# Optimization experiments

Measured on AMD Instinct MI355X. Metric: run time of the kernel, lower is better.

The kernel has to match this reference:

```python
import jax, jax.numpy as jnp
import numpy as np
from jax import lax

B, NC, NF = 16, 1024, 4096   # clouds, coarse pts/cloud, fine pts/cloud
C_IN, C_SKIP, C_HID, K = 256, 128, 256, 3
BN_EPS = 1e-5


def setup_inputs() -> dict:
    key = jax.random.key(0)
    ks = jax.random.split(key, 12)
    inp = {
        "x": jax.random.normal(ks[0], (B * NC, C_IN), jnp.float32),
        "pos": jax.random.normal(ks[1], (B * NC, 3), jnp.float32),
        "batch": jnp.arange(B * NC, dtype=jnp.int64) // NC,
        "x_skip": jax.random.normal(ks[2], (B * NF, C_SKIP), jnp.float32),
        "pos_skip": jax.random.normal(ks[3], (B * NF, 3), jnp.float32),
        "batch_skip": jnp.arange(B * NF, dtype=jnp.int64) // NF,
    }
    d_in = C_IN + C_SKIP
    inp["W1"] = jax.random.normal(ks[4], (d_in, C_HID), jnp.float32) / np.sqrt(d_in)
    inp["b1"] = jnp.zeros((C_HID,), jnp.float32)
    inp["g1"] = jnp.ones((C_HID,), jnp.float32)
    inp["be1"] = jnp.zeros((C_HID,), jnp.float32)
    inp["W2"] = jax.random.normal(ks[5], (C_HID, C_HID), jnp.float32) / np.sqrt(C_HID)
    inp["b2"] = jnp.zeros((C_HID,), jnp.float32)
    inp["g2"] = jnp.ones((C_HID,), jnp.float32)
    inp["be2"] = jnp.zeros((C_HID,), jnp.float32)
    return inp


def _knn_interpolate(x, pos, pos_skip):
    # batches are contiguous equal-size -> reshape per cloud
    xb = x.reshape(B, NC, C_IN)
    pc = pos.reshape(B, NC, 3)
    pf = pos_skip.reshape(B, NF, 3)
    # squared distances [B, NF, NC]
    d2 = jnp.sum((pf[:, :, None, :] - pc[:, None, :, :]) ** 2, axis=-1)
    neg_d, idx = lax.top_k(-d2, K)                      # [B, NF, K]
    w = 1.0 / jnp.maximum(-neg_d, 1e-16)                # inverse-squared-distance weights
    feats = xb[jnp.arange(B)[:, None, None], idx]       # [B, NF, K, C_IN]
    out = jnp.sum(w[..., None] * feats, axis=2) / jnp.sum(w, axis=2, keepdims=True)
    return out.reshape(B * NF, C_IN)


def _mlp_layer(h, W, b, g, be):
    z = jax.nn.relu(h @ W + b)
    mean = jnp.mean(z, axis=0)
    var = jnp.mean((z - mean) ** 2, axis=0)            # biased var, as torch BN
    return (z - mean) * lax.rsqrt(var + BN_EPS) * g + be


def reference(x, pos, batch, x_skip, pos_skip, batch_skip,
              W1, b1, g1, be1, W2, b2, g2, be2):
    h = _knn_interpolate(x, pos, pos_skip)
    h = jnp.concatenate([h, x_skip], axis=1)            # [B*NF, C_IN+C_SKIP]
    h = _mlp_layer(h, W1, b1, g1, be1)
    h = _mlp_layer(h, W2, b2, g2, be2)
    return h
```

## Files before the change

kernel.cpp:

```cpp
#include <hip/hip_runtime.h>
#include <hip/hip_bf16.h>
#include <hip/hip_cooperative_groups.h>

namespace cg = cooperative_groups;

#define NB    16
#define NC    1024
#define NF    4096
#define MROWS 65536
#define CIN   256
#define CSK   128
#define DIN   384
#define CHID  256
#define BN_EPS 1e-5f

typedef __attribute__((ext_vector_type(8))) short bf16x8;
typedef __attribute__((ext_vector_type(4))) float f32x4;

__device__ __forceinline__ unsigned short f2bfu(float f) {
  __hip_bfloat16 h = __float2bfloat16(f);
  return __builtin_bit_cast(unsigned short, h);
}
__device__ __forceinline__ float bfu2f(unsigned short u) {
  unsigned int w = ((unsigned int)u) << 16;
  return __builtin_bit_cast(float, w);
}

__device__ __forceinline__ void load_lds16(const void* g, void* lds) {
  __builtin_amdgcn_global_load_lds(
      (const __attribute__((address_space(1))) unsigned int*)g,
      (__attribute__((address_space(3))) unsigned int*)lds, 16, 0, 0);
}

__device__ __forceinline__ void ins3(float d2, int j, float& b0, float& b1,
                                     float& b2v, int& i0, int& i1, int& i2) {
  const bool c0 = d2 < b0, c1 = d2 < b1, c2 = d2 < b2v;
  const float nb1 = __builtin_amdgcn_fmed3f(d2, b0, b1);
  const float nb2 = __builtin_amdgcn_fmed3f(d2, b1, b2v);
  i2  = c1 ? i1 : (c2 ? j : i2);
  i1  = c0 ? i0 : (c1 ? j : i1);
  i0  = c0 ? j : i0;
  b2v = nb2;
  b1  = nb1;
  b0  = fminf(d2, b0);
}

__device__ __forceinline__ void ins3tb(float d, int j, float& b0, float& b1,
                                       float& b2v, int& i0, int& i1, int& i2) {
  const bool c0 = (d < b0) || (d == b0 && j < i0);
  const bool c1 = (d < b1) || (d == b1 && j < i1);
  const bool c2 = (d < b2v) || (d == b2v && j < i2);
  const float nb1 = __builtin_amdgcn_fmed3f(d, b0, b1);
  const float nb2 = __builtin_amdgcn_fmed3f(d, b1, b2v);
  i2  = c1 ? i1 : (c2 ? j : i2);
  i1  = c0 ? i0 : (c1 ? j : i1);
  i0  = c0 ? j : i0;
  b2v = nb2;
  b1  = nb1;
  b0  = fminf(d, b0);
}

__global__ __launch_bounds__(256) void knn_interp_kernel(
    const float* __restrict__ x,
    const float* __restrict__ pos,
    const float* __restrict__ x_skip,
    const float* __restrict__ pos_skip,
    __hip_bfloat16* __restrict__ h0,
    const float* __restrict__ W1,
    __hip_bfloat16* __restrict__ W1t,
    float* __restrict__ stats)
{
  const int tid = threadIdx.x, wid = tid >> 6, lane = tid & 63;

  if (blockIdx.x >= 2048) {
    const int c = blockIdx.x - 2048;
    if (c == 0) {
      for (int k = tid; k < 1024; k += 256) stats[k] = 0.f;
    }
    W1t[(size_t)tid * DIN + c] = __float2bfloat16(W1[(size_t)c * CHID + tid]);
    return;
  }

  __shared__ float4 cposI[NC];
  __shared__ float  fw[32][3];
  __shared__ int    fi[32][3];

  const int f0 = blockIdx.x * 32;
  const int b  = f0 >> 12;

  const float* pb = pos + (size_t)b * NC * 3;
  for (int j = tid; j < NC; j += 256) {
    cposI[((j & 127) << 3) | (j >> 7)] =
        make_float4(pb[3 * j], pb[3 * j + 1], pb[3 * j + 2], 0.f);
  }
  __syncthreads();

  const int ll = lane & 7;
  const int pl = wid * 8 + (lane >> 3);
  const int f  = f0 + pl;
  const float fx = pos_skip[(size_t)f * 3];
  const float fy = pos_skip[(size_t)f * 3 + 1];
  const float fz = pos_skip[(size_t)f * 3 + 2];
  const int jb = ll * 128;

  float a0 = 3.4e38f, a1 = 3.4e38f, a2 = 3.4e38f;
  float c0 = 3.4e38f, c1 = 3.4e38f, c2 = 3.4e38f;
  int ia0 = 0, ia1 = 0, ia2 = 0, ic0 = 0, ic1 = 0, ic2 = 0;
#pragma unroll 4
  for (int t = 0; t < 64; ++t) {
    const float4 pA = cposI[t * 8 + ll];
    const float4 pB = cposI[(t + 64) * 8 + ll];
    const float dxA = __fsub_rn(fx, pA.x), dyA = __fsub_rn(fy, pA.y),
                dzA = __fsub_rn(fz, pA.z);
    const float dxB = __fsub_rn(fx, pB.x), dyB = __fsub_rn(fy, pB.y),
                dzB = __fsub_rn(fz, pB.z);
    const float d2A = __fadd_rn(
        __fadd_rn(__fmul_rn(dxA, dxA), __fmul_rn(dyA, dyA)),
        __fmul_rn(dzA, dzA));
    const float d2B = __fadd_rn(
        __fadd_rn(__fmul_rn(dxB, dxB), __fmul_rn(dyB, dyB)),
        __fmul_rn(dzB, dzB));
    ins3(d2A, jb + t,      a0, a1, a2, ia0, ia1, ia2);
    ins3(d2B, jb + 64 + t, c0, c1, c2, ic0, ic1, ic2);
  }
  ins3(c0, ic0, a0, a1, a2, ia0, ia1, ia2);
  ins3(c1, ic1, a0, a1, a2, ia0, ia1, ia2);
  ins3(c2, ic2, a0, a1, a2, ia0, ia1, ia2);

#pragma unroll
  for (int mm = 1; mm <= 4; mm <<= 1) {
    const float o0 = __shfl_xor(a0, mm);
    const float o1 = __shfl_xor(a1, mm);
    const float o2 = __shfl_xor(a2, mm);
    const int oj0 = __shfl_xor(ia0, mm);
    const int oj1 = __shfl_xor(ia1, mm);
    const int oj2 = __shfl_xor(ia2, mm);
    ins3tb(o0, oj0, a0, a1, a2, ia0, ia1, ia2);
    ins3tb(o1, oj1, a0, a1, a2, ia0, ia1, ia2);
    ins3tb(o2, oj2, a0, a1, a2, ia0, ia1, ia2);
  }

  if (ll == 0) {
    float w0 = 1.f / fmaxf(a0, 1e-16f);
    float w1 = 1.f / fmaxf(a1, 1e-16f);
    float w2 = 1.f / fmaxf(a2, 1e-16f);
    const float inv = 1.f / (w0 + w1 + w2);
    fw[pl][0] = w0 * inv; fw[pl][1] = w1 * inv; fw[pl][2] = w2 * inv;
    fi[pl][0] = ia0; fi[pl][1] = ia1; fi[pl][2] = ia2;
  }
  __syncthreads();

  for (int pp = 0; pp < 8; ++pp) {
    const int p = wid * 8 + pp;
    const float w0 = fw[p][0], w1 = fw[p][1], w2 = fw[p][2];
    const int j0 = fi[p][0], j1 = fi[p][1], j2 = fi[p][2];
    const float4* r0 = (const float4*)(x + (size_t)(b * NC + j0) * CIN);
    const float4* r1 = (const float4*)(x + (size_t)(b * NC + j1) * CIN);
    const float4* r2 = (const float4*)(x + (size_t)(b * NC + j2) * CIN);
    const float4 a0v = r0[lane], a1v = r1[lane], a2v = r2[lane];
    float4 v;
    v.x = w0 * a0v.x + w1 * a1v.x + w2 * a2v.x;
    v.y = w0 * a0v.y + w1 * a1v.y + w2 * a2v.y;
    v.z = w0 * a0v.z + w1 * a1v.z + w2 * a2v.z;
    v.w = w0 * a0v.w + w1 * a1v.w + w2 * a2v.w;
    __hip_bfloat16* orow = h0 + (size_t)(f0 + p) * DIN;
    ushort4 o;
    o.x = f2bfu(v.x); o.y = f2bfu(v.y); o.z = f2bfu(v.z); o.w = f2bfu(v.w);
    ((ushort4*)orow)[lane] = o;
    const float2 s = ((const float2*)(x_skip + (size_t)(f0 + p) * CSK))[lane];
    const unsigned int packed =
        ((unsigned int)f2bfu(s.y) << 16) | (unsigned int)f2bfu(s.x);
    ((unsigned int*)(orow + CIN))[lane] = packed;
  }
}

__global__ __launch_bounds__(256) void prep_w2b2_kernel(
    const float* __restrict__ W2, const float* __restrict__ stats,
    const float* __restrict__ g1, const float* __restrict__ be1,
    const float* __restrict__ b2, __hip_bfloat16* __restrict__ W2t,
    float* __restrict__ b2p) {
  const int n = blockIdx.x, c = threadIdx.x;
  const int wid = c >> 6, lane = c & 63;
  const float m = stats[c] * (1.f / MROWS);
  const float var = stats[256 + c] * (1.f / MROWS) - m * m;
  const float sc = g1[c] * rsqrtf(var + BN_EPS);
  const float sh = be1[c] - m * sc;
  const float w = W2[(size_t)c * CHID + n];
  W2t[(size_t)n * CHID + c] = __float2bfloat16(sc * w);
  float p = sh * w;
#pragma unroll
  for (int off = 32; off > 0; off >>= 1) p += __shfl_down(p, off);
  __shared__ float red4[4];
  if (lane == 0) red4[wid] = p;
  __syncthreads();
  if (c == 0) b2p[n] = red4[0] + red4[1] + red4[2] + red4[3] + b2[n];
}

template<int KD>
__global__ __launch_bounds__(512) void gemm_bias_relu(
    const __hip_bfloat16* __restrict__ A,
    const __hip_bfloat16* __restrict__ Bt,
    const float* __restrict__ bias,
    __hip_bfloat16* __restrict__ out,
    float* __restrict__ gsum,
    float* __restrict__ gsq)
{
  __shared__ __hip_bfloat16 As[2 * 128 * 32];
  __shared__ __hip_bfloat16 Bs[2 * 256 * 32];
  __shared__ float ssum[256], ssq[256];
  const int tid = threadIdx.x;
  const int wid = tid >> 6, lane = tid & 63;
  const int bm = blockIdx.x;
  const int wr = wid >> 2, wc = wid & 3;
  const int la = lane & 15, lk = lane >> 4;

  if (tid < 256) { ssum[tid] = 0.f; ssq[tid] = 0.f; }

  f32x4 acc[4][4] = {};

  const int rA = tid >> 2;
  const int c8 = (tid & 3) * 8;
  const __hip_bfloat16* gA  = A  + (size_t)(bm * 128 + rA) * KD + c8;
  const __hip_bfloat16* gB0 = Bt + (size_t)rA * KD + c8;
  const __hip_bfloat16* gB1 = Bt + (size_t)(128 + rA) * KD + c8;
  char* ldsA  = (char*)As + wid * 1024;
  char* ldsB0 = (char*)Bs + wid * 1024;

  load_lds16(gA,  ldsA);
  load_lds16(gB0, ldsB0);
  load_lds16(gB1, ldsB0 + 8192);
  __syncthreads();

  const int nIter = KD / 32;
  for (int it = 0; it < nIter; ++it) {
    const int cur = it & 1, nxt = cur ^ 1;
    if (it + 1 < nIter) {
      const int k1 = (it + 1) * 32;
      load_lds16(gA  + k1, ldsA  + nxt * 8192);
      load_lds16(gB0 + k1, ldsB0 + nxt * 16384);
      load_lds16(gB1 + k1, ldsB0 + nxt * 16384 + 8192);
    }
    const __hip_bfloat16* Acur = As + cur * 4096;
    const __hip_bfloat16* Bcur = Bs + cur * 8192;
    bf16x8 af[4], bfr[4];
#pragma unroll
    for (int m = 0; m < 4; ++m)
      af[m] = *(const bf16x8*)(Acur + (wr * 64 + m * 16 + la) * 32 + lk * 8);
#pragma unroll
    for (int n = 0; n < 4; ++n)
      bfr[n] = *(const bf16x8*)(Bcur + (wc * 64 + n * 16 + la) * 32 + lk * 8);
#pragma unroll
    for (int m = 0; m < 4; ++m)
#pragma unroll
      for (int n = 0; n < 4; ++n)
        acc[m][n] = __builtin_amdgcn_mfma_f32_16x16x32_bf16(
            af[m], bfr[n], acc[m][n], 0, 0, 0);
    __syncthreads();
  }

  const int rowBase = bm * 128 + wr * 64 + lk * 4;
#pragma unroll
  for (int n = 0; n < 4; ++n) {
    const int col = wc * 64 + n * 16 + la;
    const float bs = bias[col];
    float ls = 0.f, ls2 = 0.f;
#pragma unroll
    for (int m = 0; m < 4; ++m) {
      const int row = rowBase + m * 16;
#pragma unroll
      for (int j = 0; j < 4; ++j) {
        float v = acc[m][n][j] + bs;
        v = fmaxf(v, 0.f);
        ls += v; ls2 += v * v;
        out[(size_t)(row + j) * 256 + col] = __float2bfloat16(v);
      }
    }
    atomicAdd(&ssum[col], ls);
    atomicAdd(&ssq[col], ls2);
  }
  __syncthreads();
  if (tid < 256) {
    atomicAdd(&gsum[tid], ssum[tid]);
    atomicAdd(&gsq[tid], ssq[tid]);
  }
}

__device__ __forceinline__ void gemm_tile_256(
    const __hip_bfloat16* __restrict__ A, const __hip_bfloat16* __restrict__ Bt,
    int bm, __hip_bfloat16* As, __hip_bfloat16* Bs,
    int tid, int wid, int wr, int wc, int la, int lk, f32x4 (&acc)[4][4]) {
  const int rA = tid >> 2;
  const int c8 = (tid & 3) * 8;
  const __hip_bfloat16* gA  = A  + (size_t)(bm * 128 + rA) * CHID + c8;
  const __hip_bfloat16* gB0 = Bt + (size_t)rA * CHID + c8;
  const __hip_bfloat16* gB1 = Bt + (size_t)(128 + rA) * CHID + c8;
  char* ldsA  = (char*)As + wid * 1024;
  char* ldsB0 = (char*)Bs + wid * 1024;

  load_lds16(gA,  ldsA);
  load_lds16(gB0, ldsB0);
  load_lds16(gB1, ldsB0 + 8192);
  __syncthreads();

  for (int it = 0; it < CHID / 32; ++it) {
    const int cur = it & 1, nxt = cur ^ 1;
    if (it + 1 < CHID / 32) {
      const int k1 = (it + 1) * 32;
      load_lds16(gA  + k1, ldsA  + nxt * 8192);
      load_lds16(gB0 + k1, ldsB0 + nxt * 16384);
      load_lds16(gB1 + k1, ldsB0 + nxt * 16384 + 8192);
    }
    const __hip_bfloat16* Acur = As + cur * 4096;
    const __hip_bfloat16* Bcur = Bs + cur * 8192;
    bf16x8 af[4], bfr[4];
#pragma unroll
    for (int m = 0; m < 4; ++m)
      af[m] = *(const bf16x8*)(Acur + (wr * 64 + m * 16 + la) * 32 + lk * 8);
#pragma unroll
    for (int n = 0; n < 4; ++n)
      bfr[n] = *(const bf16x8*)(Bcur + (wc * 64 + n * 16 + la) * 32 + lk * 8);
#pragma unroll
    for (int m = 0; m < 4; ++m)
#pragma unroll
      for (int n = 0; n < 4; ++n)
        acc[m][n] = __builtin_amdgcn_mfma_f32_16x16x32_bf16(
            af[m], bfr[n], acc[m][n], 0, 0, 0);
    __syncthreads();
  }
}

__global__ __launch_bounds__(512, 2) void gemm2_bn_fused(
    const __hip_bfloat16* __restrict__ A,
    const __hip_bfloat16* __restrict__ Bt,
    const float* __restrict__ bias,
    float* __restrict__ gsum, float* __restrict__ gsq,
    const float* __restrict__ g2, const float* __restrict__ be2,
    float* __restrict__ out)
{
  __shared__ __hip_bfloat16 As[2 * 128 * 32];
  __shared__ __hip_bfloat16 Bs[2 * 256 * 32];
  __shared__ float ssum[256], ssq[256];
  const int tid = threadIdx.x;
  const int wid = tid >> 6, lane = tid & 63;
  const int wr = wid >> 2, wc = wid & 3;
  const int la = lane & 15, lk = lane >> 4;
  const int bmA = blockIdx.x * 2, bmB = bmA + 1;

  if (tid < 256) { ssum[tid] = 0.f; ssq[tid] = 0.f; }

  f32x4 accA[4][4] = {};
  f32x4 accB[4][4] = {};
  gemm_tile_256(A, Bt, bmA, As, Bs, tid, wid, wr, wc, la, lk, accA);
  gemm_tile_256(A, Bt, bmB, As, Bs, tid, wid, wr, wc, la, lk, accB);

#pragma unroll
  for (int n = 0; n < 4; ++n) {
    const int col = wc * 64 + n * 16 + la;
    const float bs = bias[col];
    float ls = 0.f, ls2 = 0.f;
#pragma unroll
    for (int m = 0; m < 4; ++m)
#pragma unroll
      for (int j = 0; j < 4; ++j) {
        float vA = fmaxf(accA[m][n][j] + bs, 0.f);
        float vB = fmaxf(accB[m][n][j] + bs, 0.f);
        accA[m][n][j] = vA; accB[m][n][j] = vB;
        ls += vA + vB; ls2 += vA * vA + vB * vB;
      }
    atomicAdd(&ssum[col], ls);
    atomicAdd(&ssq[col], ls2);
  }
  __syncthreads();
  if (tid < 256) {
    atomicAdd(&gsum[tid], ssum[tid]);
    atomicAdd(&gsq[tid], ssq[tid]);
  }

  cg::this_grid().sync();

#pragma unroll
  for (int n = 0; n < 4; ++n) {
    const int col = wc * 64 + n * 16 + la;
    const float m_ = gsum[col] * (1.f / MROWS);
    const float var = gsq[col] * (1.f / MROWS) - m_ * m_;
    const float sc = g2[col] * rsqrtf(var + BN_EPS);
    const float sh = be2[col] - m_ * sc;
    const int rbA = bmA * 128 + wr * 64 + lk * 4;
    const int rbB = bmB * 128 + wr * 64 + lk * 4;
#pragma unroll
    for (int m = 0; m < 4; ++m) {
#pragma unroll
      for (int j = 0; j < 4; ++j) {
        out[(size_t)(rbA + m * 16 + j) * 256 + col] = accA[m][n][j] * sc + sh;
        out[(size_t)(rbB + m * 16 + j) * 256 + col] = accB[m][n][j] * sc + sh;
      }
    }
  }
}

__global__ __launch_bounds__(256) void bn_apply_kernel(
    const __hip_bfloat16* __restrict__ Z, const float* __restrict__ stats,
    const float* __restrict__ g2, const float* __restrict__ be2,
    float* __restrict__ out) {
  __shared__ float ssc[256], ssh[256];
  const int t = threadIdx.x;
  {
    const float m = stats[t] * (1.f / MROWS);
    const float var = stats[256 + t] * (1.f / MROWS) - m * m;
    const float sc = g2[t] * rsqrtf(var + BN_EPS);
    ssc[t] = sc;
    ssh[t] = be2[t] - m * sc;
  }
  __syncthreads();
  const size_t i8 = (size_t)blockIdx.x * 256 + t;
  const uint4 raw = ((const uint4*)Z)[i8];
  const int c0 = (int)((i8 * 8) & 255);
  const float4 scA = *(const float4*)(ssc + c0);
  const float4 scB = *(const float4*)(ssc + c0 + 4);
  const float4 shA = *(const float4*)(ssh + c0);
  const float4 shB = *(const float4*)(ssh + c0 + 4);
  float4 oa, ob;
  oa.x = bfu2f((unsigned short)(raw.x & 0xffff)) * scA.x + shA.x;
  oa.y = bfu2f((unsigned short)(raw.x >> 16))    * scA.y + shA.y;
  oa.z = bfu2f((unsigned short)(raw.y & 0xffff)) * scA.z + shA.z;
  oa.w = bfu2f((unsigned short)(raw.y >> 16))    * scA.w + shA.w;
  ob.x = bfu2f((unsigned short)(raw.z & 0xffff)) * scB.x + shB.x;
  ob.y = bfu2f((unsigned short)(raw.z >> 16))    * scB.y + shB.y;
  ob.z = bfu2f((unsigned short)(raw.w & 0xffff)) * scB.z + shB.z;
  ob.w = bfu2f((unsigned short)(raw.w >> 16))    * scB.w + shB.w;
  ((float4*)(out))[i8 * 2]     = oa;
  ((float4*)(out))[i8 * 2 + 1] = ob;
}

extern "C" void kernel_launch(void* const* d_in, const int* in_sizes, int n_in,
                              void* d_out, int out_size, void* d_ws,
                              size_t ws_size, hipStream_t stream) {
  (void)in_sizes; (void)n_in; (void)out_size; (void)ws_size;
  const float* x        = (const float*)d_in[0];
  const float* pos      = (const float*)d_in[1];
  const float* x_skip   = (const float*)d_in[3];
  const float* pos_skip = (const float*)d_in[4];
  const float* W1  = (const float*)d_in[6];
  const float* b1  = (const float*)d_in[7];
  const float* g1  = (const float*)d_in[8];
  const float* be1 = (const float*)d_in[9];
  const float* W2  = (const float*)d_in[10];
  const float* b2  = (const float*)d_in[11];
  const float* g2  = (const float*)d_in[12];
  const float* be2 = (const float*)d_in[13];
  float* out = (float*)d_out;

  char* ws = (char*)d_ws;
  __hip_bfloat16* h0  = (__hip_bfloat16*)(ws);
  __hip_bfloat16* z2  = (__hip_bfloat16*)(ws);
  __hip_bfloat16* W1t = (__hip_bfloat16*)(ws + 50331648);
  __hip_bfloat16* z1  = (__hip_bfloat16*)(ws + 50528256);
  __hip_bfloat16* W2t = (__hip_bfloat16*)(ws + 84082688);
  float* b2p    = (float*)(ws + 84213760);
  float* stats  = (float*)(ws + 84214784);

  knn_interp_kernel<<<2432, 256, 0, stream>>>(x, pos, x_skip, pos_skip, h0,
                                              W1, W1t, stats);
  gemm_bias_relu<DIN><<<512, 512, 0, stream>>>(h0, W1t, b1, z1,
                                               stats, stats + 256);
  prep_w2b2_kernel<<<256, 256, 0, stream>>>(W2, stats, g1, be1, b2, W2t, b2p);

  {
    const __hip_bfloat16* a2 = z1;
    const __hip_bfloat16* bt2 = W2t;
    const float* bias2 = b2p;
    float* gsum2 = stats + 512;
    float* gsq2  = stats + 768;
    void* args[] = {(void*)&a2, (void*)&bt2, (void*)&bias2,
                    (void*)&gsum2, (void*)&gsq2,
                    (void*)&g2, (void*)&be2, (void*)&out};
    hipError_t e = hipLaunchCooperativeKernel((const void*)gemm2_bn_fused,
                                              dim3(256), dim3(512), args, 0,
                                              stream);
    if (e != hipSuccess) {
      (void)hipGetLastError();
      gemm_bias_relu<CHID><<<512, 512, 0, stream>>>(z1, W2t, b2p, z2,
                                                    stats + 512, stats + 768);
      bn_apply_kernel<<<8192, 256, 0, stream>>>(z2, stats + 512, g2, be2, out);
    }
  }
}
```

Measured before the change: 155.9 us.

## Restructure KNN gather per thread, SoA swizzled LDS, one tile per block in fused GEMM2

The KNN kernel now keeps coarse positions as swizzled SoA arrays in LDS, read as float2 pairs. Each 8-lane group gathers and writes its own fine point's interpolated row directly, dropping the shared weight/index staging and one block barrier. The cooperative GEMM2+BN kernel now handles one 128-row tile per block across 512 blocks instead of two, and stages the normalized output through LDS so it can write coalesced float4 rows instead of strided scalar stores. Launching 512 cooperative blocks needs two blocks per CU to be co-resident, which adds more LDS pressure and grid-sync participants.

```diff
diff --git a/kernel.cpp b/kernel.cpp
--- a/kernel.cpp
+++ b/kernel.cpp
@@ -24,6 +24,9 @@
 __device__ __forceinline__ float bfu2f(unsigned short u) {
   unsigned int w = ((unsigned int)u) << 16;
   return __builtin_bit_cast(float, w);
+}
+__device__ __forceinline__ unsigned int pack2(float lo, float hi) {
+  return ((unsigned int)f2bfu(hi) << 16) | (unsigned int)f2bfu(lo);
 }
 
 __device__ __forceinline__ void load_lds16(const void* g, void* lds) {
@@ -70,7 +73,7 @@
     __hip_bfloat16* __restrict__ W1t,
     float* __restrict__ stats)
 {
-  const int tid = threadIdx.x, wid = tid >> 6, lane = tid & 63;
+  const int tid = threadIdx.x, lane = tid & 63, wid = tid >> 6;
 
   if (blockIdx.x >= 2048) {
     const int c = blockIdx.x - 2048;
@@ -81,17 +84,17 @@
     return;
   }
 
-  __shared__ float4 cposI[NC];
-  __shared__ float  fw[32][3];
-  __shared__ int    fi[32][3];
+  __shared__ float xp[NC], yp[NC], zp[NC];
 
   const int f0 = blockIdx.x * 32;
   const int b  = f0 >> 12;
 
   const float* pb = pos + (size_t)b * NC * 3;
   for (int j = tid; j < NC; j += 256) {
-    cposI[((j & 127) << 3) | (j >> 7)] =
-        make_float4(pb[3 * j], pb[3 * j + 1], pb[3 * j + 2], 0.f);
+    const int s = j >> 7, cc = j & 127, t = cc >> 1, h = cc & 1;
+    const int sl = (((t << 3) | (s ^ (t & 7))) << 1) | h;
+    const float* p = pb + 3 * j;
+    xp[sl] = p[0]; yp[sl] = p[1]; zp[sl] = p[2];
   }
   __syncthreads();
 
@@ -104,28 +107,31 @@
   const int jb = ll * 128;
 
   float a0 = 3.4e38f, a1 = 3.4e38f, a2 = 3.4e38f;
-  float c0 = 3.4e38f, c1 = 3.4e38f, c2 = 3.4e38f;
-  int ia0 = 0, ia1 = 0, ia2 = 0, ic0 = 0, ic1 = 0, ic2 = 0;
-#pragma unroll 4
+  float e0 = 3.4e38f, e1 = 3.4e38f, e2 = 3.4e38f;
+  int ia0 = 0, ia1 = 0, ia2 = 0, ie0 = 0, ie1 = 0, ie2 = 0;
+#pragma unroll 8
   for (int t = 0; t < 64; ++t) {
-    const float4 pA = cposI[t * 8 + ll];
-    const float4 pB = cposI[(t + 64) * 8 + ll];
-    const float dxA = __fsub_rn(fx, pA.x), dyA = __fsub_rn(fy, pA.y),
-                dzA = __fsub_rn(fz, pA.z);
-    const float dxB = __fsub_rn(fx, pB.x), dyB = __fsub_rn(fy, pB.y),
-                dzB = __fsub_rn(fz, pB.z);
-    const float d2A = __fadd_rn(
-        __fadd_rn(__fmul_rn(dxA, dxA), __fmul_rn(dyA, dyA)),
-        __fmul_rn(dzA, dzA));
-    const float d2B = __fadd_rn(
-        __fadd_rn(__fmul_rn(dxB, dxB), __fmul_rn(dyB, dyB)),
-        __fmul_rn(dzB, dzB));
-    ins3(d2A, jb + t,      a0, a1, a2, ia0, ia1, ia2);
-    ins3(d2B, jb + 64 + t, c0, c1, c2, ic0, ic1, ic2);
-  }
-  ins3(c0, ic0, a0, a1, a2, ia0, ia1, ia2);
-  ins3(c1, ic1, a0, a1, a2, ia0, ia1, ia2);
-  ins3(c2, ic2, a0, a1, a2, ia0, ia1, ia2);
+    const int sl2 = ((t << 3) | (ll ^ (t & 7))) << 1;
+    const float2 x2 = *(const float2*)(xp + sl2);
+    const float2 y2 = *(const float2*)(yp + sl2);
+    const float2 z2 = *(const float2*)(zp + sl2);
+    const float dx0 = __fsub_rn(fx, x2.x), dy0 = __fsub_rn(fy, y2.x),
+                dz0 = __fsub_rn(fz, z2.x);
+    const float dx1 = __fsub_rn(fx, x2.y), dy1 = __fsub_rn(fy, y2.y),
+                dz1 = __fsub_rn(fz, z2.y);
+    const float d20 = __fadd_rn(
+        __fadd_rn(__fmul_rn(dx0, dx0), __fmul_rn(dy0, dy0)),
+        __fmul_rn(dz0, dz0));
+    const float d21 = __fadd_rn(
+        __fadd_rn(__fmul_rn(dx1, dx1), __fmul_rn(dy1, dy1)),
+        __fmul_rn(dz1, dz1));
+    const int j0 = jb + 2 * t;
+    ins3(d20, j0,     a0, a1, a2, ia0, ia1, ia2);
+    ins3(d21, j0 + 1, e0, e1, e2, ie0, ie1, ie2);
+  }
+  ins3tb(e0, ie0, a0, a1, a2, ia0, ia1, ia2);
+  ins3tb(e1, ie1, a0, a1, a2, ia0, ia1, ia2);
+  ins3tb(e2, ie2, a0, a1, a2, ia0, ia1, ia2);
 
 #pragma unroll
   for (int mm = 1; mm <= 4; mm <<= 1) {
@@ -140,37 +146,41 @@
     ins3tb(o2, oj2, a0, a1, a2, ia0, ia1, ia2);
   }
 
-  if (ll == 0) {
-    float w0 = 1.f / fmaxf(a0, 1e-16f);
-    float w1 = 1.f / fmaxf(a1, 1e-16f);
-    float w2 = 1.f / fmaxf(a2, 1e-16f);
-    const float inv = 1.f / (w0 + w1 + w2);
-    fw[pl][0] = w0 * inv; fw[pl][1] = w1 * inv; fw[pl][2] = w2 * inv;
-    fi[pl][0] = ia0; fi[pl][1] = ia1; fi[pl][2] = ia2;
-  }
-  __syncthreads();
-
-  for (int pp = 0; pp < 8; ++pp) {
-    const int p = wid * 8 + pp;
-    const float w0 = fw[p][0], w1 = fw[p][1], w2 = fw[p][2];
-    const int j0 = fi[p][0], j1 = fi[p][1], j2 = fi[p][2];
-    const float4* r0 = (const float4*)(x + (size_t)(b * NC + j0) * CIN);
-    const float4* r1 = (const float4*)(x + (size_t)(b * NC + j1) * CIN);
-    const float4* r2 = (const float4*)(x + (size_t)(b * NC + j2) * CIN);
-    const float4 a0v = r0[lane], a1v = r1[lane], a2v = r2[lane];
+  float w0 = 1.f / fmaxf(a0, 1e-16f);
+  float w1 = 1.f / fmaxf(a1, 1e-16f);
+  float w2 = 1.f / fmaxf(a2, 1e-16f);
+  const float inv = 1.f / (w0 + w1 + w2);
+  w0 *= inv; w1 *= inv; w2 *= inv;
+
+  const float4* r0 = (const float4*)(x + (size_t)(b * NC + ia0) * CIN);
+  const float4* r1 = (const float4*)(x + (size_t)(b * NC + ia1) * CIN);
+  const float4* r2 = (const float4*)(x + (size_t)(b * NC + ia2) * CIN);
+  __hip_bfloat16* orow = h0 + (size_t)f * DIN;
+  unsigned int* o2u = (unsigned int*)orow;
+#pragma unroll
+  for (int k = 0; k < 8; ++k) {
+    const int fi4 = k * 8 + ll;
+    const float4 A = r0[fi4], B = r1[fi4], C = r2[fi4];
     float4 v;
-    v.x = w0 * a0v.x + w1 * a1v.x + w2 * a2v.x;
-    v.y = w0 * a0v.y + w1 * a1v.y + w2 * a2v.y;
-    v.z = w0 * a0v.z + w1 * a1v.z + w2 * a2v.z;
-    v.w = w0 * a0v.w + w1 * a1v.w + w2 * a2v.w;
-    __hip_bfloat16* orow = h0 + (size_t)(f0 + p) * DIN;
-    ushort4 o;
-    o.x = f2bfu(v.x); o.y = f2bfu(v.y); o.z = f2bfu(v.z); o.w = f2bfu(v.w);
-    ((ushort4*)orow)[lane] = o;
-    const float2 s = ((const float2*)(x_skip + (size_t)(f0 + p) * CSK))[lane];
-    const unsigned int packed =
-        ((unsigned int)f2bfu(s.y) << 16) | (unsigned int)f2bfu(s.x);
-    ((unsigned int*)(orow + CIN))[lane] = packed;
+    v.x = w0 * A.x + w1 * B.x + w2 * C.x;
+    v.y = w0 * A.y + w1 * B.y + w2 * C.y;
+    v.z = w0 * A.z + w1 * B.z + w2 * C.z;
+    v.w = w0 * A.w + w1 * B.w + w2 * C.w;
+    uint2 o;
+    o.x = pack2(v.x, v.y);
+    o.y = pack2(v.z, v.w);
+    ((uint2*)o2u)[fi4] = o;
+  }
+  const float4* xs = (const float4*)(x_skip + (size_t)f * CSK);
+  unsigned int* o2s = (unsigned int*)(orow + CIN);
+#pragma unroll
+  for (int k = 0; k < 4; ++k) {
+    const int fi4 = k * 8 + ll;
+    const float4 s = xs[fi4];
+    uint2 o;
+    o.x = pack2(s.x, s.y);
+    o.y = pack2(s.z, s.w);
+    ((uint2*)o2s)[fi4] = o;
   }
 }
 
@@ -285,50 +295,6 @@
   }
 }
 
-__device__ __forceinline__ void gemm_tile_256(
-    const __hip_bfloat16* __restrict__ A, const __hip_bfloat16* __restrict__ Bt,
-    int bm, __hip_bfloat16* As, __hip_bfloat16* Bs,
-    int tid, int wid, int wr, int wc, int la, int lk, f32x4 (&acc)[4][4]) {
-  const int rA = tid >> 2;
-  const int c8 = (tid & 3) * 8;
-  const __hip_bfloat16* gA  = A  + (size_t)(bm * 128 + rA) * CHID + c8;
-  const __hip_bfloat16* gB0 = Bt + (size_t)rA * CHID + c8;
-  const __hip_bfloat16* gB1 = Bt + (size_t)(128 + rA) * CHID + c8;
-  char* ldsA  = (char*)As + wid * 1024;
-  char* ldsB0 = (char*)Bs + wid * 1024;
-
-  load_lds16(gA,  ldsA);
-  load_lds16(gB0, ldsB0);
-  load_lds16(gB1, ldsB0 + 8192);
-  __syncthreads();
-
-  for (int it = 0; it < CHID / 32; ++it) {
-    const int cur = it & 1, nxt = cur ^ 1;
-    if (it + 1 < CHID / 32) {
-      const int k1 = (it + 1) * 32;
-      load_lds16(gA  + k1, ldsA  + nxt * 8192);
-      load_lds16(gB0 + k1, ldsB0 + nxt * 16384);
-      load_lds16(gB1 + k1, ldsB0 + nxt * 16384 + 8192);
-    }
-    const __hip_bfloat16* Acur = As + cur * 4096;
-    const __hip_bfloat16* Bcur = Bs + cur * 8192;
-    bf16x8 af[4], bfr[4];
-#pragma unroll
-    for (int m = 0; m < 4; ++m)
-      af[m] = *(const bf16x8*)(Acur + (wr * 64 + m * 16 + la) * 32 + lk * 8);
-#pragma unroll
-    for (int n = 0; n < 4; ++n)
-      bfr[n] = *(const bf16x8*)(Bcur + (wc * 64 + n * 16 + la) * 32 + lk * 8);
-#pragma unroll
-    for (int m = 0; m < 4; ++m)
-#pragma unroll
-      for (int n = 0; n < 4; ++n)
-        acc[m][n] = __builtin_amdgcn_mfma_f32_16x16x32_bf16(
-            af[m], bfr[n], acc[m][n], 0, 0, 0);
-    __syncthreads();
-  }
-}
-
 __global__ __launch_bounds__(512, 2) void gemm2_bn_fused(
     const __hip_bfloat16* __restrict__ A,
     const __hip_bfloat16* __restrict__ Bt,
@@ -337,21 +303,59 @@
     const float* __restrict__ g2, const float* __restrict__ be2,
     float* __restrict__ out)
 {
-  __shared__ __hip_bfloat16 As[2 * 128 * 32];
-  __shared__ __hip_bfloat16 Bs[2 * 256 * 32];
-  __shared__ float ssum[256], ssq[256];
+  __shared__ __align__(16) char smem[51200];
+  __hip_bfloat16* As = (__hip_bfloat16*)smem;
+  __hip_bfloat16* Bs = (__hip_bfloat16*)(smem + 16384);
+  float* ssum = (float*)(smem + 49152);
+  float* ssq  = (float*)(smem + 50176);
   const int tid = threadIdx.x;
   const int wid = tid >> 6, lane = tid & 63;
+  const int bm = blockIdx.x;
   const int wr = wid >> 2, wc = wid & 3;
   const int la = lane & 15, lk = lane >> 4;
-  const int bmA = blockIdx.x * 2, bmB = bmA + 1;
 
   if (tid < 256) { ssum[tid] = 0.f; ssq[tid] = 0.f; }
 
-  f32x4 accA[4][4] = {};
-  f32x4 accB[4][4] = {};
-  gemm_tile_256(A, Bt, bmA, As, Bs, tid, wid, wr, wc, la, lk, accA);
-  gemm_tile_256(A, Bt, bmB, As, Bs, tid, wid, wr, wc, la, lk, accB);
+  f32x4 acc[4][4] = {};
+
+  const int rA = tid >> 2;
+  const int c8 = (tid & 3) * 8;
+  const __hip_bfloat16* gA  = A  + (size_t)(bm * 128 + rA) * CHID + c8;
+  const __hip_bfloat16* gB0 = Bt + (size_t)rA * CHID + c8;
+  const __hip_bfloat16* gB1 = Bt + (size_t)(128 + rA) * CHID + c8;
+  char* ldsA  = (char*)As + wid * 1024;
+  char* ldsB0 = (char*)Bs + wid * 1024;
+
+  load_lds16(gA,  ldsA);
+  load_lds16(gB0, ldsB0);
+  load_lds16(gB1, ldsB0 + 8192);
+  __syncthreads();
+
+  for (int it = 0; it < CHID / 32; ++it) {
+    const int cur = it & 1, nxt = cur ^ 1;
+    if (it + 1 < CHID / 32) {
+      const int k1 = (it + 1) * 32;
+      load_lds16(gA  + k1, ldsA  + nxt * 8192);
+      load_lds16(gB0 + k1, ldsB0 + nxt * 16384);
+      load_lds16(gB1 + k1, ldsB0 + nxt * 16384 + 8192);
+    }
+    const __hip_bfloat16* Acur = As + cur * 4096;
+    const __hip_bfloat16* Bcur = Bs + cur * 8192;
+    bf16x8 af[4], bfr[4];
+#pragma unroll
+    for (int m = 0; m < 4; ++m)
+      af[m] = *(const bf16x8*)(Acur + (wr * 64 + m * 16 + la) * 32 + lk * 8);
+#pragma unroll
+    for (int n = 0; n < 4; ++n)
+      bfr[n] = *(const bf16x8*)(Bcur + (wc * 64 + n * 16 + la) * 32 + lk * 8);
+#pragma unroll
+    for (int m = 0; m < 4; ++m)
+#pragma unroll
+      for (int n = 0; n < 4; ++n)
+        acc[m][n] = __builtin_amdgcn_mfma_f32_16x16x32_bf16(
+            af[m], bfr[n], acc[m][n], 0, 0, 0);
+    __syncthreads();
+  }
 
 #pragma unroll
   for (int n = 0; n < 4; ++n) {
@@ -362,10 +366,9 @@
     for (int m = 0; m < 4; ++m)
 #pragma unroll
       for (int j = 0; j < 4; ++j) {
-        float vA = fmaxf(accA[m][n][j] + bs, 0.f);
-        float vB = fmaxf(accB[m][n][j] + bs, 0.f);
-        accA[m][n][j] = vA; accB[m][n][j] = vB;
-        ls += vA + vB; ls2 += vA * vA + vB * vB;
+        const float v = fmaxf(acc[m][n][j] + bs, 0.f);
+        acc[m][n][j] = v;
+        ls += v; ls2 += v * v;
       }
     atomicAdd(&ssum[col], ls);
     atomicAdd(&ssq[col], ls2);
@@ -378,23 +381,47 @@
 
   cg::this_grid().sync();
 
-#pragma unroll
-  for (int n = 0; n < 4; ++n) {
-    const int col = wc * 64 + n * 16 + la;
-    const float m_ = gsum[col] * (1.f / MROWS);
-    const float var = gsq[col] * (1.f / MROWS) - m_ * m_;
-    const float sc = g2[col] * rsqrtf(var + BN_EPS);
-    const float sh = be2[col] - m_ * sc;
-    const int rbA = bmA * 128 + wr * 64 + lk * 4;
-    const int rbB = bmB * 128 + wr * 64 + lk * 4;
-#pragma unroll
-    for (int m = 0; m < 4; ++m) {
-#pragma unroll
-      for (int j = 0; j < 4; ++j) {
-        out[(size_t)(rbA + m * 16 + j) * 256 + col] = accA[m][n][j] * sc + sh;
-        out[(size_t)(rbB + m * 16 + j) * 256 + col] = accB[m][n][j] * sc + sh;
+  if (tid < 256) {
+    const float m_ = gsum[tid] * (1.f / MROWS);
+    const float var = gsq[tid] * (1.f / MROWS) - m_ * m_;
+    const float sc = g2[tid] * rsqrtf(var + BN_EPS);
+    ssum[tid] = sc;
+    ssq[tid]  = be2[tid] - m_ * sc;
+  }
+  __syncthreads();
+
+  float* stage = (float*)smem;
+#pragma unroll
+  for (int ch = 0; ch < 4; ++ch) {
+    if (wr == (ch >> 1)) {
+#pragma unroll
+      for (int mm2 = 0; mm2 < 2; ++mm2) {
+        const int m = (ch & 1) * 2 + mm2;
+#pragma unroll
+        for (int n = 0; n < 4; ++n) {
+          const int col = wc * 64 + n * 16 + la;
+#pragma unroll
+          for (int j = 0; j < 4; ++j)
+            stage[(mm2 * 16 + lk * 4 + j) * 256 + col] = acc[m][n][j];
+        }
       }
     }
+    __syncthreads();
+#pragma unroll
+    for (int k = 0; k < 4; ++k) {
+      const int f4 = k * 512 + tid;
+      const int row = f4 >> 6;
+      const int col = (f4 & 63) * 4;
+      float4 v = *(const float4*)(stage + row * 256 + col);
+      const float4 sc4 = *(const float4*)(ssum + col);
+      const float4 sh4 = *(const float4*)(ssq + col);
+      v.x = v.x * sc4.x + sh4.x;
+      v.y = v.y * sc4.y + sh4.y;
+      v.z = v.z * sc4.z + sh4.z;
+      v.w = v.w * sc4.w + sh4.w;
+      *(float4*)(out + (size_t)(bm * 128 + ch * 32 + row) * 256 + col) = v;
+    }
+    __syncthreads();
   }
 }
 
@@ -475,7 +502,7 @@
                     (void*)&gsum2, (void*)&gsq2,
                     (void*)&g2, (void*)&be2, (void*)&out};
     hipError_t e = hipLaunchCooperativeKernel((const void*)gemm2_bn_fused,
-                                              dim3(256), dim3(512), args, 0,
+                                              dim3(512), dim3(512), args, 0,
                                               stream);
     if (e != hipSuccess) {
       (void)hipGetLastError();
```

After: 178.8 us. +14.7%, slower.
